# Kernel optimization log

Hardware: AMD Instinct MI355X
Metric: run time of the kernel (lower is better)

## Reference

```python
import jax, jax.numpy as jnp
import numpy as np

B, C, D, W, H = 4, 256, 32, 32, 32  # img_dim = D, in_channels = C, model_num = 4


def setup_inputs() -> dict:
    key = jax.random.key(0)
    ks = jax.random.split(key, 8)
    s = 0.02
    inp = {
        "m1": jax.random.normal(ks[0], (B, C, D, W, H), jnp.float32),
        "m2": jax.random.normal(ks[1], (B, C, D, W, H), jnp.float32),
        "m3": jax.random.normal(ks[2], (B, C, D, W, H), jnp.float32),
        "m4": jax.random.normal(ks[3], (B, C, D, W, H), jnp.float32),
        # nn.Linear weights (torch convention: y = x @ W.T + b)
        "Wq": jax.random.normal(ks[4], (D, D), jnp.float32) * s,
        "bq": jnp.zeros((D,), jnp.float32),
        "Wk": jax.random.normal(ks[5], (D, D), jnp.float32) * s,
        "bk": jnp.zeros((D,), jnp.float32),
        # four 1x1x1 Conv3d kernels, squeezed to [model, out_c, in_c]
        "Wc": jax.random.normal(ks[6], (4, C, C), jnp.float32) * s,
        "bc": jnp.zeros((4, C), jnp.float32),
    }
    return inp


def reference(m1, m2, m3, m4, Wq, bq, Wk, bk, Wc, bc):
    d = m1.shape[2]
    # adaptive_avg_pool3d(x, (D,1,1)) == mean over W,H -> [B,C,D]; stack 4 modalities -> [B,C,4,D]
    pooled = jnp.stack([m.mean(axis=(3, 4)) for m in (m1, m2, m3, m4)], axis=2)
    q = jnp.einsum('bcd,ed->bce', pooled[:, :, 0], Wq) + bq          # [B,C,D]
    k = jnp.einsum('bcmd,ed->bcme', pooled, Wk) + bk                 # [B,C,4,D]
    # per-modality attention logits: q . k_m over D -> [B,C,4]
    a = jnp.einsum('bcd,bcmd->bcm', q, k) / jnp.sqrt(jnp.float32(d))
    a = jax.nn.softmax(a, axis=-1)                                   # [B,C,4]
    ms = jnp.stack([m1, m2, m3, m4], axis=0)                         # [4,B,C,D,W,H]
    # 1x1x1 Conv3d == channel-mixing GEMM per voxel
    conv = jnp.einsum('mbcdwh,moc->mbodwh', ms, Wc) + bc[:, None, :, None, None, None]
    # weighted sum of the 4 conv outputs by per-(B,C) attention weights
    out = jnp.einsum('bcm,mbcdwh->bcdwh', a, conv)                   # [B,C,D,W,H]
    return out
```

## Files before the change

### kernel.cpp

```cpp
#include <hip/hip_runtime.h>
#include <hip/hip_bf16.h>

#define NB 4
#define NC 256
#define ND 32
#define WH 1024
#define DWH 32768
#define KTOT 1024

typedef __attribute__((ext_vector_type(8))) short short8;
typedef __attribute__((ext_vector_type(4))) float f32x4;

static __device__ __forceinline__ unsigned short f32_to_bf16(float f) {
    unsigned u = __builtin_bit_cast(unsigned, f);
    u = u + 0x7fff + ((u >> 16) & 1);
    return (unsigned short)(u >> 16);
}

__global__ __launch_bounds__(256) void pool_kernel(
    const float* __restrict__ i0, const float* __restrict__ i1,
    const float* __restrict__ i2, const float* __restrict__ i3,
    float* __restrict__ pooled)
{
    int bid = blockIdx.x;
    int m   = bid & 3;
    int bc  = bid >> 2;
    const float* src = (m == 0 ? i0 : m == 1 ? i1 : m == 2 ? i2 : i3)
                       + (size_t)bc * DWH;
    int t = threadIdx.x;
    int wave = t >> 6, lane = t & 63;

    for (int d = wave; d < ND; d += 4) {
        const float4* row = (const float4*)(src + (size_t)d * WH);
        float s = 0.f;
        #pragma unroll
        for (int j = 0; j < 4; ++j) {
            float4 v = row[lane + 64 * j];
            s += v.x + v.y + v.z + v.w;
        }
        #pragma unroll
        for (int off = 32; off; off >>= 1) s += __shfl_down(s, off, 64);
        if (lane == 0) pooled[bc * 128 + m * 32 + d] = s * (1.0f / 1024.0f);
    }
}

__global__ __launch_bounds__(64) void attn_kernel(
    const float* __restrict__ pooled,
    const float* __restrict__ Wq, const float* __restrict__ bq,
    const float* __restrict__ Wk, const float* __restrict__ bk,
    const float* __restrict__ Wc, const float* __restrict__ bcv,
    unsigned short* __restrict__ Amat, float* __restrict__ beff)
{
    int bc_idx = blockIdx.x;
    int lane = threadIdx.x;
    int e = lane & 31;
    const float* P = pooled + bc_idx * 128;

    float q = 0.f, kv[4] = {0.f, 0.f, 0.f, 0.f};
    for (int d = 0; d < 32; ++d) {
        float pq = P[d];
        float wq = Wq[e * 32 + d], wk = Wk[e * 32 + d];
        q += pq * wq;
        #pragma unroll
        for (int m = 0; m < 4; ++m) kv[m] += P[m * 32 + d] * wk;
    }
    q += bq[e];
    #pragma unroll
    for (int m = 0; m < 4; ++m) kv[m] += bk[e];

    float lg[4];
    #pragma unroll
    for (int m = 0; m < 4; ++m) {
        float p = q * kv[m];
        #pragma unroll
        for (int off = 16; off; off >>= 1) p += __shfl_xor(p, off, 32);
        lg[m] = p * 0.17677669529663687f;
    }
    float mx = fmaxf(fmaxf(lg[0], lg[1]), fmaxf(lg[2], lg[3]));
    float ex[4], s = 0.f;
    #pragma unroll
    for (int m = 0; m < 4; ++m) { ex[m] = __expf(lg[m] - mx); s += ex[m]; }
    float a[4];
    #pragma unroll
    for (int m = 0; m < 4; ++m) a[m] = ex[m] / s;

    int c = bc_idx & 255;
    if (lane == 0) {
        float be = 0.f;
        #pragma unroll
        for (int m = 0; m < 4; ++m) be += a[m] * bcv[m * NC + c];
        beff[bc_idx] = be;
    }
    unsigned short* Arow = Amat + (size_t)bc_idx * KTOT;
    #pragma unroll
    for (int j = 0; j < 16; ++j) {
        int k = j * 64 + lane;
        int m = k >> 8, cin = k & 255;
        float v = a[m] * Wc[(m * NC + c) * NC + cin];
        Arow[k] = f32_to_bf16(v);
    }
}

#define BM 128
#define BN 128
#define BK 64

static __device__ __forceinline__ int swz(int row, int chunk) {
    return row * 64 + ((chunk ^ (row & 7)) << 3);
}

__global__ __launch_bounds__(256, 3) void gemm_kernel(
    const float* __restrict__ i0, const float* __restrict__ i1,
    const float* __restrict__ i2, const float* __restrict__ i3,
    const unsigned short* __restrict__ Amat,
    const float* __restrict__ beff,
    float* __restrict__ out)
{
    __shared__ __align__(16) short As[BM * BK];
    __shared__ __align__(16) short Bs[BN * BK];

    int raw = blockIdx.x;
    int sb  = (raw & 7) * 256 + (raw >> 3);
    int ot = sb & 1;
    int xt = (sb >> 1) & 255;
    int b  = sb >> 9;
    int o0 = ot * BM, x0 = xt * BN;

    const unsigned short* Ab = Amat + ((size_t)b * NC + o0) * KTOT;

    int t = threadIdx.x;
    int wave = t >> 6, lane = t & 63;
    int wr = wave >> 1, wc = wave & 1;
    int lrow = lane & 15, lk = lane >> 4;

    f32x4 acc[4][4];
    #pragma unroll
    for (int mi = 0; mi < 4; ++mi)
        #pragma unroll
        for (int ni = 0; ni < 4; ++ni)
            acc[mi][ni] = (f32x4){0.f, 0.f, 0.f, 0.f};

    int xq = t & 31;
    int kb = (t >> 5) * 8;

    int ar = wave * 32 + (lane >> 3);
    int aq = (lane & 7) ^ (lane >> 3);
    const unsigned short* asrc = Ab + (size_t)ar * KTOT + aq * 8;

    float4 v[8];
    {
        const float* Bb = i0 + (size_t)b * NC * DWH + x0;
        #pragma unroll
        for (int j = 0; j < 8; ++j)
            v[j] = *(const float4*)(Bb + (size_t)(kb + j) * DWH + xq * 4);
    }

    for (int it = 0; it < KTOT / BK; ++it) {
        int k0 = it * BK;

        __syncthreads();

        #pragma unroll
        for (int p = 0; p < 4; ++p)
            __builtin_amdgcn_global_load_lds(
                (const __attribute__((address_space(1))) unsigned int*)
                    (asrc + (size_t)p * 8 * KTOT + k0),
                (__attribute__((address_space(3))) unsigned int*)
                    (As + (wave * 32 + p * 8) * 64),
                16, 0, 0);

        #pragma unroll
        for (int i = 0; i < 4; ++i) {
            short8 pk;
            #pragma unroll
            for (int j = 0; j < 8; ++j)
                pk[j] = (short)f32_to_bf16(((const float*)&v[j])[i]);
            int xl = xq * 4 + i;
            *(short8*)(&Bs[swz(xl, t >> 5)]) = pk;
        }

        __syncthreads();

        if (it + 1 < KTOT / BK) {
            int itn = it + 1;
            int m  = itn >> 2;
            int cbase = (itn & 3) * 64;
            const float* Bb = (m == 0 ? i0 : m == 1 ? i1 : m == 2 ? i2 : i3)
                              + ((size_t)b * NC + cbase) * DWH + x0;
            #pragma unroll
            for (int j = 0; j < 8; ++j)
                v[j] = *(const float4*)(Bb + (size_t)(kb + j) * DWH + xq * 4);
        }

        #pragma unroll
        for (int kk = 0; kk < 2; ++kk) {
            int q = kk * 4 + lk;
            short8 af[4], bf[4];
            #pragma unroll
            for (int mi = 0; mi < 4; ++mi) {
                int r = wr * 64 + mi * 16 + lrow;
                af[mi] = *(const short8*)(&As[swz(r, q)]);
            }
            #pragma unroll
            for (int ni = 0; ni < 4; ++ni) {
                int x = wc * 64 + ni * 16 + lrow;
                bf[ni] = *(const short8*)(&Bs[swz(x, q)]);
            }
            #pragma unroll
            for (int mi = 0; mi < 4; ++mi)
                #pragma unroll
                for (int ni = 0; ni < 4; ++ni)
                    acc[mi][ni] = __builtin_amdgcn_mfma_f32_16x16x32_bf16(
                        af[mi], bf[ni], acc[mi][ni], 0, 0, 0);
        }
    }

    const float* beff_b = beff + b * NC + o0;
    float* outb = out + ((size_t)b * NC + o0) * DWH + x0;
    #pragma unroll
    for (int mi = 0; mi < 4; ++mi) {
        #pragma unroll
        for (int r4 = 0; r4 < 4; ++r4) {
            int row = wr * 64 + mi * 16 + lk * 4 + r4;
            float bias = beff_b[row];
            float* orow = outb + (size_t)row * DWH;
            #pragma unroll
            for (int ni = 0; ni < 4; ++ni) {
                int col = wc * 64 + ni * 16 + lrow;
                orow[col] = acc[mi][ni][r4] + bias;
            }
        }
    }
}

extern "C" void kernel_launch(void* const* d_in, const int* in_sizes, int n_in,
                              void* d_out, int out_size, void* d_ws, size_t ws_size,
                              hipStream_t stream) {
    const float* m1 = (const float*)d_in[0];
    const float* m2 = (const float*)d_in[1];
    const float* m3 = (const float*)d_in[2];
    const float* m4 = (const float*)d_in[3];
    const float* Wq = (const float*)d_in[4];
    const float* bq = (const float*)d_in[5];
    const float* Wk = (const float*)d_in[6];
    const float* bk = (const float*)d_in[7];
    const float* Wc = (const float*)d_in[8];
    const float* bcv = (const float*)d_in[9];
    float* out = (float*)d_out;

    float* pooled        = (float*)d_ws;
    unsigned short* Amat = (unsigned short*)((char*)d_ws + 524288);
    float* beff          = (float*)((char*)d_ws + 524288 + 2097152);

    pool_kernel<<<NB * NC * 4, 256, 0, stream>>>(m1, m2, m3, m4, pooled);
    attn_kernel<<<NB * NC, 64, 0, stream>>>(pooled, Wq, bq, Wk, bk, Wc, bcv,
                                            Amat, beff);
    gemm_kernel<<<(NB) * (NC / BM) * (DWH / BN), 256, 0, stream>>>(
        m1, m2, m3, m4, Amat, beff, out);
}
```

Before: 264.9 us.

## Double-buffer GEMM LDS tiles with two-stage register prefetch and one barrier

```diff
diff --git a/kernel.cpp b/kernel.cpp
--- a/kernel.cpp
+++ b/kernel.cpp
@@ -15,6 +15,10 @@
     unsigned u = __builtin_bit_cast(unsigned, f);
     u = u + 0x7fff + ((u >> 16) & 1);
     return (unsigned short)(u >> 16);
+}
+
+static __device__ __forceinline__ unsigned pack_bf16x2(float lo, float hi) {
+    return (unsigned)f32_to_bf16(lo) | ((unsigned)f32_to_bf16(hi) << 16);
 }
 
 __global__ __launch_bounds__(256) void pool_kernel(
@@ -109,15 +113,15 @@
     return row * 64 + ((chunk ^ (row & 7)) << 3);
 }
 
-__global__ __launch_bounds__(256, 3) void gemm_kernel(
+__global__ __launch_bounds__(256, 2) void gemm_kernel(
     const float* __restrict__ i0, const float* __restrict__ i1,
     const float* __restrict__ i2, const float* __restrict__ i3,
     const unsigned short* __restrict__ Amat,
     const float* __restrict__ beff,
     float* __restrict__ out)
 {
-    __shared__ __align__(16) short As[BM * BK];
-    __shared__ __align__(16) short Bs[BN * BK];
+    __shared__ __align__(16) short As[2 * BM * BK];
+    __shared__ __align__(16) short Bs[2 * BN * BK];
 
     int raw = blockIdx.x;
     int sb  = (raw & 7) * 256 + (raw >> 3);
@@ -148,50 +152,88 @@
     const unsigned short* asrc = Ab + (size_t)ar * KTOT + aq * 8;
 
     float4 v[8];
+
     {
         const float* Bb = i0 + (size_t)b * NC * DWH + x0;
         #pragma unroll
         for (int j = 0; j < 8; ++j)
             v[j] = *(const float4*)(Bb + (size_t)(kb + j) * DWH + xq * 4);
-    }
-
-    for (int it = 0; it < KTOT / BK; ++it) {
-        int k0 = it * BK;
-
-        __syncthreads();
-
         #pragma unroll
         for (int p = 0; p < 4; ++p)
             __builtin_amdgcn_global_load_lds(
                 (const __attribute__((address_space(1))) unsigned int*)
-                    (asrc + (size_t)p * 8 * KTOT + k0),
+                    (asrc + (size_t)p * 8 * KTOT),
                 (__attribute__((address_space(3))) unsigned int*)
                     (As + (wave * 32 + p * 8) * 64),
                 16, 0, 0);
-
+        __builtin_amdgcn_sched_barrier(0);
+        uint4 pk[4];
         #pragma unroll
         for (int i = 0; i < 4; ++i) {
-            short8 pk;
-            #pragma unroll
-            for (int j = 0; j < 8; ++j)
-                pk[j] = (short)f32_to_bf16(((const float*)&v[j])[i]);
-            int xl = xq * 4 + i;
-            *(short8*)(&Bs[swz(xl, t >> 5)]) = pk;
-        }
-
-        __syncthreads();
-
-        if (it + 1 < KTOT / BK) {
-            int itn = it + 1;
-            int m  = itn >> 2;
-            int cbase = (itn & 3) * 64;
+            unsigned w[4];
+            #pragma unroll
+            for (int j = 0; j < 4; ++j)
+                w[j] = pack_bf16x2(((const float*)&v[2 * j])[i],
+                                   ((const float*)&v[2 * j + 1])[i]);
+            pk[i] = (uint4){w[0], w[1], w[2], w[3]};
+        }
+        const float* Bb1 = i0 + ((size_t)b * NC + 64) * DWH + x0;
+        #pragma unroll
+        for (int j = 0; j < 8; ++j)
+            v[j] = *(const float4*)(Bb1 + (size_t)(kb + j) * DWH + xq * 4);
+        __builtin_amdgcn_sched_barrier(0);
+        #pragma unroll
+        for (int i = 0; i < 4; ++i)
+            *(uint4*)(&Bs[swz(xq * 4 + i, t >> 5)]) = pk[i];
+        asm volatile("s_waitcnt vmcnt(8) lgkmcnt(0)" ::: "memory");
+        __builtin_amdgcn_s_barrier();
+        __builtin_amdgcn_sched_barrier(0);
+    }
+
+    int cur = 0;
+    for (int it = 0; it < KTOT / BK; ++it) {
+        int itn  = (it < 15) ? it + 1 : 15;
+        int itn2 = (it < 14) ? it + 2 : 15;
+        short* Asw = As + (cur ^ 1) * (BM * BK);
+        short* Bsw = Bs + (cur ^ 1) * (BN * BK);
+
+        #pragma unroll
+        for (int p = 0; p < 4; ++p)
+            __builtin_amdgcn_global_load_lds(
+                (const __attribute__((address_space(1))) unsigned int*)
+                    (asrc + (size_t)p * 8 * KTOT + itn * BK),
+                (__attribute__((address_space(3))) unsigned int*)
+                    (Asw + (wave * 32 + p * 8) * 64),
+                16, 0, 0);
+        __builtin_amdgcn_sched_barrier(0);
+
+        uint4 pk[4];
+        #pragma unroll
+        for (int i = 0; i < 4; ++i) {
+            unsigned w[4];
+            #pragma unroll
+            for (int j = 0; j < 4; ++j)
+                w[j] = pack_bf16x2(((const float*)&v[2 * j])[i],
+                                   ((const float*)&v[2 * j + 1])[i]);
+            pk[i] = (uint4){w[0], w[1], w[2], w[3]};
+        }
+
+        {
+            int m = itn2 >> 2, cbase = (itn2 & 3) * 64;
             const float* Bb = (m == 0 ? i0 : m == 1 ? i1 : m == 2 ? i2 : i3)
                               + ((size_t)b * NC + cbase) * DWH + x0;
             #pragma unroll
             for (int j = 0; j < 8; ++j)
                 v[j] = *(const float4*)(Bb + (size_t)(kb + j) * DWH + xq * 4);
         }
-
+        __builtin_amdgcn_sched_barrier(0);
+
+        #pragma unroll
+        for (int i = 0; i < 4; ++i)
+            *(uint4*)(&Bsw[swz(xq * 4 + i, t >> 5)]) = pk[i];
+
+        const short* Asr = As + cur * (BM * BK);
+        const short* Bsr = Bs + cur * (BN * BK);
         #pragma unroll
         for (int kk = 0; kk < 2; ++kk) {
             int q = kk * 4 + lk;
@@ -199,20 +241,27 @@
             #pragma unroll
             for (int mi = 0; mi < 4; ++mi) {
                 int r = wr * 64 + mi * 16 + lrow;
-                af[mi] = *(const short8*)(&As[swz(r, q)]);
+                af[mi] = *(const short8*)(&Asr[swz(r, q)]);
             }
             #pragma unroll
             for (int ni = 0; ni < 4; ++ni) {
                 int x = wc * 64 + ni * 16 + lrow;
-                bf[ni] = *(const short8*)(&Bs[swz(x, q)]);
+                bf[ni] = *(const short8*)(&Bsr[swz(x, q)]);
             }
+            __builtin_amdgcn_s_setprio(1);
             #pragma unroll
             for (int mi = 0; mi < 4; ++mi)
                 #pragma unroll
                 for (int ni = 0; ni < 4; ++ni)
                     acc[mi][ni] = __builtin_amdgcn_mfma_f32_16x16x32_bf16(
                         af[mi], bf[ni], acc[mi][ni], 0, 0, 0);
-        }
+            __builtin_amdgcn_s_setprio(0);
+        }
+
+        asm volatile("s_waitcnt vmcnt(8) lgkmcnt(0)" ::: "memory");
+        __builtin_amdgcn_s_barrier();
+        __builtin_amdgcn_sched_barrier(0);
+        cur ^= 1;
     }
 
     const float* beff_b = beff + b * NC + o0;
```

Result: no change. 267.5 us (+1.0%).

## Hand-schedule GEMM main loop with raw barriers, partial waitcnt and MFMA priority

Applied to the files above, without the earlier changes.

```diff
diff --git a/kernel.cpp b/kernel.cpp
--- a/kernel.cpp
+++ b/kernel.cpp
@@ -15,6 +15,10 @@
     unsigned u = __builtin_bit_cast(unsigned, f);
     u = u + 0x7fff + ((u >> 16) & 1);
     return (unsigned short)(u >> 16);
+}
+
+static __device__ __forceinline__ unsigned pack_bf16x2(float lo, float hi) {
+    return (unsigned)f32_to_bf16(lo) | ((unsigned)f32_to_bf16(hi) << 16);
 }
 
 __global__ __launch_bounds__(256) void pool_kernel(
@@ -148,6 +152,7 @@
     const unsigned short* asrc = Ab + (size_t)ar * KTOT + aq * 8;
 
     float4 v[8];
+
     {
         const float* Bb = i0 + (size_t)b * NC * DWH + x0;
         #pragma unroll
@@ -155,42 +160,50 @@
             v[j] = *(const float4*)(Bb + (size_t)(kb + j) * DWH + xq * 4);
     }
 
+    #pragma unroll 1
     for (int it = 0; it < KTOT / BK; ++it) {
-        int k0 = it * BK;
-
-        __syncthreads();
+        __builtin_amdgcn_s_barrier();
+        __builtin_amdgcn_sched_barrier(0);
 
         #pragma unroll
         for (int p = 0; p < 4; ++p)
             __builtin_amdgcn_global_load_lds(
                 (const __attribute__((address_space(1))) unsigned int*)
-                    (asrc + (size_t)p * 8 * KTOT + k0),
+                    (asrc + (size_t)p * 8 * KTOT + it * BK),
                 (__attribute__((address_space(3))) unsigned int*)
                     (As + (wave * 32 + p * 8) * 64),
                 16, 0, 0);
-
+        __builtin_amdgcn_sched_barrier(0);
+
+        uint4 pk[4];
         #pragma unroll
         for (int i = 0; i < 4; ++i) {
-            short8 pk;
-            #pragma unroll
-            for (int j = 0; j < 8; ++j)
-                pk[j] = (short)f32_to_bf16(((const float*)&v[j])[i]);
-            int xl = xq * 4 + i;
-            *(short8*)(&Bs[swz(xl, t >> 5)]) = pk;
-        }
-
-        __syncthreads();
-
-        if (it + 1 < KTOT / BK) {
-            int itn = it + 1;
-            int m  = itn >> 2;
-            int cbase = (itn & 3) * 64;
+            unsigned w[4];
+            #pragma unroll
+            for (int j = 0; j < 4; ++j)
+                w[j] = pack_bf16x2(((const float*)&v[2 * j])[i],
+                                   ((const float*)&v[2 * j + 1])[i]);
+            pk[i] = (uint4){w[0], w[1], w[2], w[3]};
+        }
+
+        {
+            int itn = (it < 15) ? it + 1 : 15;
+            int m = itn >> 2, cbase = (itn & 3) * 64;
             const float* Bb = (m == 0 ? i0 : m == 1 ? i1 : m == 2 ? i2 : i3)
                               + ((size_t)b * NC + cbase) * DWH + x0;
             #pragma unroll
             for (int j = 0; j < 8; ++j)
                 v[j] = *(const float4*)(Bb + (size_t)(kb + j) * DWH + xq * 4);
         }
+        __builtin_amdgcn_sched_barrier(0);
+
+        #pragma unroll
+        for (int i = 0; i < 4; ++i)
+            *(uint4*)(&Bs[swz(xq * 4 + i, t >> 5)]) = pk[i];
+
+        asm volatile("s_waitcnt vmcnt(8) lgkmcnt(0)" ::: "memory");
+        __builtin_amdgcn_s_barrier();
+        __builtin_amdgcn_sched_barrier(0);
 
         #pragma unroll
         for (int kk = 0; kk < 2; ++kk) {
@@ -206,12 +219,14 @@
                 int x = wc * 64 + ni * 16 + lrow;
                 bf[ni] = *(const short8*)(&Bs[swz(x, q)]);
             }
+            __builtin_amdgcn_s_setprio(1);
             #pragma unroll
             for (int mi = 0; mi < 4; ++mi)
                 #pragma unroll
                 for (int ni = 0; ni < 4; ++ni)
                     acc[mi][ni] = __builtin_amdgcn_mfma_f32_16x16x32_bf16(
                         af[mi], bf[ni], acc[mi][ni], 0, 0, 0);
+            __builtin_amdgcn_s_setprio(0);
         }
     }
 
```

New measurement: 263.2 us. Within noise of the previous version (-0.6%).

## Double-buffer A tile and prefetch B two iterations ahead in GEMM

Applied to the files above, without the earlier changes.

```diff
diff --git a/kernel.cpp b/kernel.cpp
--- a/kernel.cpp
+++ b/kernel.cpp
@@ -15,6 +15,10 @@
     unsigned u = __builtin_bit_cast(unsigned, f);
     u = u + 0x7fff + ((u >> 16) & 1);
     return (unsigned short)(u >> 16);
+}
+
+static __device__ __forceinline__ unsigned pack_bf16x2(float lo, float hi) {
+    return (unsigned)f32_to_bf16(lo) | ((unsigned)f32_to_bf16(hi) << 16);
 }
 
 __global__ __launch_bounds__(256) void pool_kernel(
@@ -109,6 +113,70 @@
     return row * 64 + ((chunk ^ (row & 7)) << 3);
 }
 
+#define GEMM_ITER(J, VC, ARD, AWR)                                            \
+  {                                                                           \
+    __builtin_amdgcn_s_barrier();               \
+    __builtin_amdgcn_sched_barrier(0);                                        \
+    int ja_ = ((J) + 1 < 16) ? (J) + 1 : 15;                                  \
+    _Pragma("unroll")                                                         \
+    for (int p_ = 0; p_ < 4; ++p_)                                            \
+      __builtin_amdgcn_global_load_lds(                                       \
+          (const __attribute__((address_space(1))) unsigned int*)             \
+              (asrc + (size_t)p_ * 8 * KTOT + ja_ * BK),                      \
+          (__attribute__((address_space(3))) unsigned int*)                   \
+              ((AWR) + (wave * 32 + p_ * 8) * 64),                            \
+          16, 0, 0);                                                          \
+    __builtin_amdgcn_sched_barrier(0);                                        \
+    uint4 pk_[4];                              \
+    _Pragma("unroll")                                                         \
+    for (int i_ = 0; i_ < 4; ++i_) {                                          \
+      unsigned w0_ = pack_bf16x2(((const float*)&(VC)[0])[i_],                \
+                                 ((const float*)&(VC)[1])[i_]);               \
+      unsigned w1_ = pack_bf16x2(((const float*)&(VC)[2])[i_],                \
+                                 ((const float*)&(VC)[3])[i_]);               \
+      unsigned w2_ = pack_bf16x2(((const float*)&(VC)[4])[i_],                \
+                                 ((const float*)&(VC)[5])[i_]);               \
+      unsigned w3_ = pack_bf16x2(((const float*)&(VC)[6])[i_],                \
+                                 ((const float*)&(VC)[7])[i_]);               \
+      pk_[i_] = (uint4){w0_, w1_, w2_, w3_};                                  \
+    }                                                                         \
+    {                                                 \
+      int jb_ = ((J) + 2 < 16) ? (J) + 2 : 15;                                \
+      int m_ = jb_ >> 2, cb_ = (jb_ & 3) * 64;                                \
+      const float* Bb_ = (m_ == 0 ? i0 : m_ == 1 ? i1 : m_ == 2 ? i2 : i3)    \
+                         + ((size_t)b * NC + cb_) * DWH + x0;                 \
+      _Pragma("unroll")                                                       \
+      for (int j_ = 0; j_ < 8; ++j_)                                          \
+        (VC)[j_] = *(const float4*)(Bb_ + (size_t)(kb + j_) * DWH + xq * 4);  \
+    }                                                                         \
+    __builtin_amdgcn_sched_barrier(0);                                        \
+    _Pragma("unroll")                                                         \
+    for (int i_ = 0; i_ < 4; ++i_)                                            \
+      *(uint4*)(&Bs[swz(xq * 4 + i_, t >> 5)]) = pk_[i_];                     \
+    asm volatile("s_waitcnt vmcnt(20) lgkmcnt(0)" ::: "memory");              \
+    __builtin_amdgcn_s_barrier();               \
+    __builtin_amdgcn_sched_barrier(0);                                        \
+    _Pragma("unroll")                                                         \
+    for (int kk_ = 0; kk_ < 2; ++kk_) {                                       \
+      int q_ = kk_ * 4 + lk;                                                  \
+      short8 af_[4], bf_[4];                                                  \
+      _Pragma("unroll")                                                       \
+      for (int mi_ = 0; mi_ < 4; ++mi_)                                       \
+        af_[mi_] = *(const short8*)(&(ARD)[swz(wr * 64 + mi_ * 16 + lrow, q_)]); \
+      _Pragma("unroll")                                                       \
+      for (int ni_ = 0; ni_ < 4; ++ni_)                                       \
+        bf_[ni_] = *(const short8*)(&Bs[swz(wc * 64 + ni_ * 16 + lrow, q_)]); \
+      __builtin_amdgcn_s_setprio(1);                                          \
+      _Pragma("unroll")                                                       \
+      for (int mi_ = 0; mi_ < 4; ++mi_)                                       \
+        _Pragma("unroll")                                                     \
+        for (int ni_ = 0; ni_ < 4; ++ni_)                                     \
+          acc[mi_][ni_] = __builtin_amdgcn_mfma_f32_16x16x32_bf16(            \
+              af_[mi_], bf_[ni_], acc[mi_][ni_], 0, 0, 0);                    \
+      __builtin_amdgcn_s_setprio(0);                                          \
+    }                                                                         \
+  }
+
 __global__ __launch_bounds__(256, 3) void gemm_kernel(
     const float* __restrict__ i0, const float* __restrict__ i1,
     const float* __restrict__ i2, const float* __restrict__ i3,
@@ -116,7 +184,7 @@
     const float* __restrict__ beff,
     float* __restrict__ out)
 {
-    __shared__ __align__(16) short As[BM * BK];
+    __shared__ __align__(16) short As[2 * BM * BK];
     __shared__ __align__(16) short Bs[BN * BK];
 
     int raw = blockIdx.x;
@@ -147,72 +215,35 @@
     int aq = (lane & 7) ^ (lane >> 3);
     const unsigned short* asrc = Ab + (size_t)ar * KTOT + aq * 8;
 
-    float4 v[8];
+    short* As0 = As;
+    short* As1 = As + BM * BK;
+
+    float4 va[8], vb[8];
+
     {
         const float* Bb = i0 + (size_t)b * NC * DWH + x0;
         #pragma unroll
         for (int j = 0; j < 8; ++j)
-            v[j] = *(const float4*)(Bb + (size_t)(kb + j) * DWH + xq * 4);
-    }
-
-    for (int it = 0; it < KTOT / BK; ++it) {
-        int k0 = it * BK;
-
-        __syncthreads();
-
+            va[j] = *(const float4*)(Bb + (size_t)(kb + j) * DWH + xq * 4);
         #pragma unroll
         for (int p = 0; p < 4; ++p)
             __builtin_amdgcn_global_load_lds(
                 (const __attribute__((address_space(1))) unsigned int*)
-                    (asrc + (size_t)p * 8 * KTOT + k0),
+                    (asrc + (size_t)p * 8 * KTOT),
                 (__attribute__((address_space(3))) unsigned int*)
-                    (As + (wave * 32 + p * 8) * 64),
+                    (As0 + (wave * 32 + p * 8) * 64),
                 16, 0, 0);
-
-        #pragma unroll
-        for (int i = 0; i < 4; ++i) {
-            short8 pk;
-            #pragma unroll
-            for (int j = 0; j < 8; ++j)
-                pk[j] = (short)f32_to_bf16(((const float*)&v[j])[i]);
-            int xl = xq * 4 + i;
-            *(short8*)(&Bs[swz(xl, t >> 5)]) = pk;
-        }
-
-        __syncthreads();
-
-        if (it + 1 < KTOT / BK) {
-            int itn = it + 1;
-            int m  = itn >> 2;
-            int cbase = (itn & 3) * 64;
-            const float* Bb = (m == 0 ? i0 : m == 1 ? i1 : m == 2 ? i2 : i3)
-                              + ((size_t)b * NC + cbase) * DWH + x0;
-            #pragma unroll
-            for (int j = 0; j < 8; ++j)
-                v[j] = *(const float4*)(Bb + (size_t)(kb + j) * DWH + xq * 4);
-        }
-
-        #pragma unroll
-        for (int kk = 0; kk < 2; ++kk) {
-            int q = kk * 4 + lk;
-            short8 af[4], bf[4];
-            #pragma unroll
-            for (int mi = 0; mi < 4; ++mi) {
-                int r = wr * 64 + mi * 16 + lrow;
-                af[mi] = *(const short8*)(&As[swz(r, q)]);
-            }
-            #pragma unroll
-            for (int ni = 0; ni < 4; ++ni) {
-                int x = wc * 64 + ni * 16 + lrow;
-                bf[ni] = *(const short8*)(&Bs[swz(x, q)]);
-            }
-            #pragma unroll
-            for (int mi = 0; mi < 4; ++mi)
-                #pragma unroll
-                for (int ni = 0; ni < 4; ++ni)
-                    acc[mi][ni] = __builtin_amdgcn_mfma_f32_16x16x32_bf16(
-                        af[mi], bf[ni], acc[mi][ni], 0, 0, 0);
-        }
+        const float* Bb1 = i0 + ((size_t)b * NC + 64) * DWH + x0;
+        #pragma unroll
+        for (int j = 0; j < 8; ++j)
+            vb[j] = *(const float4*)(Bb1 + (size_t)(kb + j) * DWH + xq * 4);
+    }
+
+    #pragma unroll 1
+    for (int it2 = 0; it2 < 8; ++it2) {
+        int it = it2 * 2;
+        GEMM_ITER(it,     va, As0, As1);
+        GEMM_ITER(it + 1, vb, As1, As0);
     }
 
     const float* beff_b = beff + b * NC + o0;
```

Measured after the change: 684.5 us. 2.58x slower.
